# Kernel tuning notes

Hardware: AMD Instinct MI355X
Metric: run time of the kernel (lower is better)

## Reference

```python
import jax, jax.numpy as jnp
import numpy as np

GROUP = 128  # int4 quant group size and Hadamard block size

# Sylvester Hadamard matrix of size 128, orthonormal (H @ H.T = I)
_h = np.array([[1.0]], dtype=np.float32)
while _h.shape[0] < GROUP:
    _h = np.kron(_h, np.array([[1.0, 1.0], [1.0, -1.0]], dtype=np.float32))
H128 = jnp.asarray(_h / np.sqrt(GROUP))


def hadamard_rotate(x):
    # blockwise Hadamard rotation along the last dim (last dim % 128 == 0)
    *lead, n = x.shape
    xr = x.reshape(*lead, n // GROUP, GROUP) @ H128
    return xr.reshape(*lead, n)


def dequant_int4(wq, scales):
    # wq: [out, in] uint4 values in [0,16); scales: [out, in//GROUP]
    out_dim, in_dim = wq.shape
    w = (wq.astype(jnp.float32) - 8.0).reshape(out_dim, in_dim // GROUP, GROUP)
    w = w * scales[:, :, None]
    return w.reshape(out_dim, in_dim)


def rotate_linear_int4(x, wq, scales):
    # y = hadamard(x) @ dequant(W).T
    return hadamard_rotate(x) @ dequant_int4(wq, scales).T


def setup_inputs() -> dict:
    key = jax.random.key(0)
    ks = jax.random.split(key, 7)
    T, D, I = 4096, 4096, 12288  # tokens, hidden, intermediate
    x = jax.random.normal(ks[0], (T, D), dtype=jnp.float32)
    wq_gate = jax.random.randint(ks[1], (I, D), 0, 16, dtype=jnp.int32)
    s_gate = jax.random.uniform(ks[2], (I, D // GROUP), dtype=jnp.float32) * 0.01
    wq_up = jax.random.randint(ks[3], (I, D), 0, 16, dtype=jnp.int32)
    s_up = jax.random.uniform(ks[4], (I, D // GROUP), dtype=jnp.float32) * 0.01
    wq_down = jax.random.randint(ks[5], (D, I), 0, 16, dtype=jnp.int32)
    s_down = jax.random.uniform(ks[6], (D, I // GROUP), dtype=jnp.float32) * 0.01
    return {"x": x, "wq_gate": wq_gate, "s_gate": s_gate,
            "wq_up": wq_up, "s_up": s_up,
            "wq_down": wq_down, "s_down": s_down}


def reference(x, wq_gate, s_gate, wq_up, s_up, wq_down, s_down):
    gate = rotate_linear_int4(x, wq_gate, s_gate)   # [T, I]
    up = rotate_linear_int4(x, wq_up, s_up)         # [T, I]
    h = jax.nn.silu(gate) * up                       # SiluAndMul on cat([gate, up])
    return rotate_linear_int4(h, wq_down, s_down)    # [T, D]
```

## Files before the change

kernel.cpp:

```cpp
#include <hip/hip_runtime.h>
#include <hip/hip_bf16.h>
#include <cstdint>

#define T_DIM 4096
#define D_DIM 4096
#define I_DIM 12288
#define GRP   128

typedef __attribute__((ext_vector_type(8))) short bf16x8;
typedef __attribute__((ext_vector_type(4))) float f32x4;
typedef __attribute__((ext_vector_type(4))) int   int32x4;

typedef __attribute__((address_space(3))) void lds_void;
typedef const __attribute__((address_space(1))) void gmem_void;

static __device__ __forceinline__ unsigned short f2bf(float f) {
    unsigned int u = __float_as_uint(f);
    u += 0x7FFFu + ((u >> 16) & 1u);
    return (unsigned short)(u >> 16);
}
static __device__ __forceinline__ float bf2f(unsigned short b) {
    return __uint_as_float(((unsigned int)b) << 16);
}

__global__ void had_f32_to_bf16(const float* __restrict__ in, unsigned short* __restrict__ out,
                                int ngroups) {
    int gid = blockIdx.x * (blockDim.x >> 6) + (threadIdx.x >> 6);
    if (gid >= ngroups) return;
    int lane = threadIdx.x & 63;
    const float2 v2 = *reinterpret_cast<const float2*>(in + (size_t)gid * 128 + lane * 2);
    float v0 = v2.x, v1 = v2.y;
    { float t0 = v0 + v1, t1 = v0 - v1; v0 = t0; v1 = t1; }
#pragma unroll
    for (int m = 1; m <= 32; m <<= 1) {
        float b0 = __shfl_xor(v0, m);
        float b1 = __shfl_xor(v1, m);
        if (lane & m) { v0 = b0 - v0; v1 = b1 - v1; }
        else          { v0 = v0 + b0; v1 = v1 + b1; }
    }
    const float s = 0.08838834764831843f;
    unsigned int o = (unsigned int)f2bf(v0 * s) | ((unsigned int)f2bf(v1 * s) << 16);
    *reinterpret_cast<unsigned int*>(out + (size_t)gid * 128 + lane * 2) = o;
}

__global__ void had_bf16_inplace(unsigned short* __restrict__ buf, int ngroups) {
    int gid = blockIdx.x * (blockDim.x >> 6) + (threadIdx.x >> 6);
    if (gid >= ngroups) return;
    int lane = threadIdx.x & 63;
    unsigned int pv = *reinterpret_cast<const unsigned int*>(buf + (size_t)gid * 128 + lane * 2);
    float v0 = __uint_as_float((pv & 0xFFFFu) << 16);
    float v1 = __uint_as_float(pv & 0xFFFF0000u);
    { float t0 = v0 + v1, t1 = v0 - v1; v0 = t0; v1 = t1; }
#pragma unroll
    for (int m = 1; m <= 32; m <<= 1) {
        float b0 = __shfl_xor(v0, m);
        float b1 = __shfl_xor(v1, m);
        if (lane & m) { v0 = b0 - v0; v1 = b1 - v1; }
        else          { v0 = v0 + b0; v1 = v1 + b1; }
    }
    const float s = 0.08838834764831843f;
    unsigned int o = (unsigned int)f2bf(v0 * s) | ((unsigned int)f2bf(v1 * s) << 16);
    *reinterpret_cast<unsigned int*>(buf + (size_t)gid * 128 + lane * 2) = o;
}

__global__ void dequant_w(const int* __restrict__ Wq, const float* __restrict__ S,
                          unsigned short* __restrict__ Wbf, int In, int total8) {
    int t = blockIdx.x * blockDim.x + threadIdx.x;
    if (t >= total8) return;
    size_t base = (size_t)t * 8;
    size_t row = base / (size_t)In;
    int col = (int)(base - row * (size_t)In);
    float sc = S[row * (size_t)(In >> 7) + (col >> 7)];
    const int32x4* p = reinterpret_cast<const int32x4*>(Wq + base);
    int32x4 a = p[0], b = p[1];
    float nsc = -8.0f * sc;
    unsigned int o0 = (unsigned int)f2bf((float)a.x * sc + nsc) |
                      ((unsigned int)f2bf((float)a.y * sc + nsc) << 16);
    unsigned int o1 = (unsigned int)f2bf((float)a.z * sc + nsc) |
                      ((unsigned int)f2bf((float)a.w * sc + nsc) << 16);
    unsigned int o2 = (unsigned int)f2bf((float)b.x * sc + nsc) |
                      ((unsigned int)f2bf((float)b.y * sc + nsc) << 16);
    unsigned int o3 = (unsigned int)f2bf((float)b.z * sc + nsc) |
                      ((unsigned int)f2bf((float)b.w * sc + nsc) << 16);
    *reinterpret_cast<uint4*>(Wbf + base) = make_uint4(o0, o1, o2, o3);
}


#define GBAR()  __builtin_amdgcn_s_barrier()
#define FENCE() asm volatile("" ::: "memory")
#define VMW(n)  asm volatile("s_waitcnt vmcnt(" #n ")" ::: "memory")
#define P1()    __builtin_amdgcn_s_setprio(1)
#define P0()    __builtin_amdgcn_s_setprio(0)

#define STG(src, row0, base, h, kb)                                                    \
  { _Pragma("unroll")                                                                  \
    for (int i_ = 0; i_ < 2; ++i_) {                                                   \
      const int rl_ = (h) * 128 + i_ * 64 + (tid >> 3);                                \
      const int gs_ = (tid & 7) ^ ((tid >> 3) & 7);                                    \
      const unsigned short* gp_ = (src) + (size_t)((row0) + rl_) * K + (kb) + gs_ * 8; \
      unsigned short* lp_ = lds + (base) + ((h) * 128 + i_ * 64 + wid * 8) * 64;       \
      __builtin_amdgcn_global_load_lds((gmem_void*)gp_, (lds_void*)lp_, 16, 0, 0);     \
    } }

#define LDA(base, q)                                                                   \
  _Pragma("unroll")                                                                    \
  for (int mi_ = 0; mi_ < 2; ++mi_)                                                    \
  _Pragma("unroll")                                                                    \
  for (int ks_ = 0; ks_ < 2; ++ks_) {                                                  \
    int r_ = wr * 128 + (q) * 32 + mi_ * 16 + (lane & 15);                             \
    int c_ = ks_ * 4 + kc;                                                             \
    af[mi_][ks_] = *reinterpret_cast<const bf16x8*>(                                   \
        lds + (base) + r_ * 64 + ((c_ ^ (r_ & 7)) << 3));                              \
  }

#define LDB(base)                                                                      \
  _Pragma("unroll")                                                                    \
  for (int ni_ = 0; ni_ < 4; ++ni_)                                                    \
  _Pragma("unroll")                                                                    \
  for (int ks_ = 0; ks_ < 2; ++ks_) {                                                  \
    int r_ = wc * 64 + ni_ * 16 + (lane & 15);                                         \
    int c_ = ks_ * 4 + kc;                                                             \
    bk[ni_][ks_] = *reinterpret_cast<const bf16x8*>(                                   \
        lds + (base) + r_ * 64 + ((c_ ^ (r_ & 7)) << 3));                              \
  }

#define MF16(q)                                                                        \
  _Pragma("unroll")                                                                    \
  for (int ks_ = 0; ks_ < 2; ++ks_)                                                    \
  _Pragma("unroll")                                                                    \
  for (int mi_ = 0; mi_ < 2; ++mi_)                                                    \
  _Pragma("unroll")                                                                    \
  for (int ni_ = 0; ni_ < 4; ++ni_)                                                    \
    acc[(q) * 2 + mi_][ni_] = __builtin_amdgcn_mfma_f32_16x16x32_bf16(                 \
        af[mi_][ks_], bk[ni_][ks_], acc[(q) * 2 + mi_][ni_], 0, 0, 0);

#define B0_ 49152
#define B1_ 65536

template<int MODE>
__global__ __launch_bounds__(512, 2)
void gemm256(const unsigned short* __restrict__ A,
             const unsigned short* __restrict__ W,
             void* __restrict__ C, int M, int N, int K)
{
    __shared__ __align__(16) unsigned short lds[81920];

    const int MT = M >> 8;
    const int nwg = gridDim.x;
    const int bid = blockIdx.x;
    const int cpx = nwg >> 3;
    const int wg  = (bid & 7) * cpx + (bid >> 3);
    const int m0 = (wg % MT) << 8;
    const int n0 = (wg / MT) << 8;

    const int tid  = threadIdx.x;
    const int lane = tid & 63;
    const int wid  = tid >> 6;
    const int wr = wid >> 2;
    const int wc = wid & 3;
    const int kc = lane >> 4;

    f32x4 acc[8][4];
#pragma unroll
    for (int i = 0; i < 8; ++i)
#pragma unroll
        for (int j = 0; j < 4; ++j) acc[i][j] = (f32x4)0.0f;

    const int NT = K >> 6;
    const int J  = NT >> 1;

    STG(A, m0, 0,     0, 0);  STG(A, m0, 0,     1, 0);
    STG(W, n0, B0_,   0, 0);  STG(W, n0, B0_,   1, 0);
    STG(A, m0, 16384, 0, 64); STG(A, m0, 16384, 1, 64);
    STG(W, n0, B1_,   0, 64);
    VMW(6);
    GBAR(); FENCE();

    int ra = 0, rb = 1, rc = 2;

    for (int j = 0; j < J; ++j) {
        const bool st = (j < J - 1);
        const int a   = j << 1;
        const int kT1 = (a + 1) << 6;
        const int kT2 = (a + 2) << 6;
        const int kT3 = (a + 3) << 6;
        const int baA = ra << 14, bbA = rb << 14, bcA = rc << 14;
        bf16x8 af[2][2], bk[4][2];

        STG(W, n0, B1_, 1, kT1);
        LDB(B0_); LDA(baA, 0);
        P1(); MF16(0); P0(); GBAR(); FENCE();
        if (st) STG(A, m0, bcA, 0, kT2);
        LDA(baA, 1);
        P1(); MF16(1); P0(); GBAR(); FENCE();
        if (st) STG(W, n0, B0_, 0, kT2);
        LDA(baA, 2);
        P1(); MF16(2); P0(); GBAR(); FENCE();
        if (st) STG(W, n0, B0_, 1, kT2);
        LDA(baA, 3);
        P1(); MF16(3); P0();
        if (st) { VMW(6); } else { VMW(0); }
        GBAR(); FENCE();
        if (st) STG(A, m0, bcA, 1, kT2);
        LDB(B1_); LDA(bbA, 0);
        P1(); MF16(0); P0(); GBAR(); FENCE();
        if (st) STG(A, m0, baA, 0, kT3);
        LDA(bbA, 1);
        P1(); MF16(1); P0(); GBAR(); FENCE();
        if (st) STG(A, m0, baA, 1, kT3);
        LDA(bbA, 2);
        P1(); MF16(2); P0(); GBAR(); FENCE();
        if (st) STG(W, n0, B1_, 0, kT3);
        LDA(bbA, 3);
        P1(); MF16(3); P0();
        if (st) { VMW(6); }
        GBAR(); FENCE();
        int t_ = ra; ra = rc; rc = rb; rb = t_;
    }

#pragma unroll
    for (int mi = 0; mi < 8; ++mi)
#pragma unroll
        for (int ni = 0; ni < 4; ++ni) {
            const int col = n0 + (wc << 6) + ni * 16 + (lane & 15);
#pragma unroll
            for (int r = 0; r < 4; ++r) {
                const int row = m0 + (wr << 7) + mi * 16 + ((lane >> 4) << 2) + r;
                const size_t idx = (size_t)row * N + col;
                if (MODE == 2) {
                    ((float*)C)[idx] = acc[mi][ni][r];
                } else if (MODE == 0) {
                    ((unsigned short*)C)[idx] = f2bf(acc[mi][ni][r]);
                } else {
                    float g = bf2f(((unsigned short*)C)[idx]);
                    float u = acc[mi][ni][r];
                    float h = (g / (1.0f + __expf(-g))) * u;
                    ((unsigned short*)C)[idx] = f2bf(h);
                }
            }
        }
}

__global__ __launch_bounds__(256, 2)
void gemm_gateup_fb(const unsigned short* __restrict__ Xr,
                    const int* __restrict__ Wg, const float* __restrict__ Sg,
                    const int* __restrict__ Wu, const float* __restrict__ Su,
                    unsigned short* __restrict__ H)
{
    __shared__ __align__(16) unsigned short lA [128 * 64];
    __shared__ __align__(16) unsigned short lBg[128 * 64];
    __shared__ __align__(16) unsigned short lBu[128 * 64];
    const int MT = T_DIM / 128;
    const int bid = blockIdx.x;
    const int m0 = (bid % MT) * 128;
    const int n0 = (bid / MT) * 128;
    const int tid  = threadIdx.x;
    const int lane = tid & 63;
    const int wid  = tid >> 6;
    const int wr = wid >> 1, wc = wid & 1;
    f32x4 accG[4][4], accU[4][4];
#pragma unroll
    for (int i = 0; i < 4; ++i)
#pragma unroll
        for (int j = 0; j < 4; ++j) { accG[i][j] = (f32x4)0.0f; accU[i][j] = (f32x4)0.0f; }
    const int arow = lane >> 3;
    const int acol = (lane & 7) * 8;
    const int SStride = D_DIM / GRP;
    for (int k0 = 0; k0 < D_DIM; k0 += 64) {
        __syncthreads();
#pragma unroll
        for (int it = 0; it < 4; ++it) {
            int chunk = wid * 4 + it;
            const unsigned short* gp = Xr + (size_t)(m0 + chunk * 8 + arow) * D_DIM + k0 + acol;
            __builtin_amdgcn_global_load_lds((gmem_void*)gp, (lds_void*)(lA + chunk * 512), 16, 0, 0);
        }
        const int g = k0 >> 7;
#pragma unroll
        for (int i = 0; i < 8; ++i) {
            int linear = i * 1024 + tid * 4;
            int r = linear >> 6;
            int c = linear & 63;
            const int32x4 wg = *reinterpret_cast<const int32x4*>(Wg + (size_t)(n0 + r) * D_DIM + k0 + c);
            const int32x4 wu = *reinterpret_cast<const int32x4*>(Wu + (size_t)(n0 + r) * D_DIM + k0 + c);
            float scg = Sg[(size_t)(n0 + r) * SStride + g];
            float scu = Su[(size_t)(n0 + r) * SStride + g];
            unsigned int g01 = (unsigned int)f2bf((float)(wg.x - 8) * scg) | ((unsigned int)f2bf((float)(wg.y - 8) * scg) << 16);
            unsigned int g23 = (unsigned int)f2bf((float)(wg.z - 8) * scg) | ((unsigned int)f2bf((float)(wg.w - 8) * scg) << 16);
            unsigned int u01 = (unsigned int)f2bf((float)(wu.x - 8) * scu) | ((unsigned int)f2bf((float)(wu.y - 8) * scu) << 16);
            unsigned int u23 = (unsigned int)f2bf((float)(wu.z - 8) * scu) | ((unsigned int)f2bf((float)(wu.w - 8) * scu) << 16);
            *reinterpret_cast<uint2*>(lBg + r * 64 + c) = make_uint2(g01, g23);
            *reinterpret_cast<uint2*>(lBu + r * 64 + c) = make_uint2(u01, u23);
        }
        __syncthreads();
#pragma unroll
        for (int ks = 0; ks < 2; ++ks) {
            const int koff = ks * 32 + (lane >> 4) * 8;
            bf16x8 af[4], bg[4], bu[4];
#pragma unroll
            for (int mi = 0; mi < 4; ++mi)
                af[mi] = *reinterpret_cast<const bf16x8*>(lA + (wr * 64 + mi * 16 + (lane & 15)) * 64 + koff);
#pragma unroll
            for (int ni = 0; ni < 4; ++ni) {
                bg[ni] = *reinterpret_cast<const bf16x8*>(lBg + (wc * 64 + ni * 16 + (lane & 15)) * 64 + koff);
                bu[ni] = *reinterpret_cast<const bf16x8*>(lBu + (wc * 64 + ni * 16 + (lane & 15)) * 64 + koff);
            }
#pragma unroll
            for (int mi = 0; mi < 4; ++mi)
#pragma unroll
                for (int ni = 0; ni < 4; ++ni) {
                    accG[mi][ni] = __builtin_amdgcn_mfma_f32_16x16x32_bf16(af[mi], bg[ni], accG[mi][ni], 0, 0, 0);
                    accU[mi][ni] = __builtin_amdgcn_mfma_f32_16x16x32_bf16(af[mi], bu[ni], accU[mi][ni], 0, 0, 0);
                }
        }
    }
#pragma unroll
    for (int mi = 0; mi < 4; ++mi)
#pragma unroll
        for (int ni = 0; ni < 4; ++ni) {
            const int col = n0 + wc * 64 + ni * 16 + (lane & 15);
#pragma unroll
            for (int r = 0; r < 4; ++r) {
                const int row = m0 + wr * 64 + mi * 16 + (lane >> 4) * 4 + r;
                float gv = accG[mi][ni][r];
                float uv = accU[mi][ni][r];
                float hv = (gv / (1.0f + __expf(-gv))) * uv;
                H[(size_t)row * I_DIM + col] = f2bf(hv);
            }
        }
}

__global__ __launch_bounds__(256, 2)
void gemm_down_fb(const unsigned short* __restrict__ Hr,
                  const int* __restrict__ Wd, const float* __restrict__ Sd,
                  float* __restrict__ Out)
{
    __shared__ __align__(16) unsigned short lA[128 * 64];
    __shared__ __align__(16) unsigned short lB[128 * 64];
    const int MT = T_DIM / 128;
    const int bid = blockIdx.x;
    const int m0 = (bid % MT) * 128;
    const int n0 = (bid / MT) * 128;
    const int tid  = threadIdx.x;
    const int lane = tid & 63;
    const int wid  = tid >> 6;
    const int wr = wid >> 1, wc = wid & 1;
    f32x4 acc[4][4];
#pragma unroll
    for (int i = 0; i < 4; ++i)
#pragma unroll
        for (int j = 0; j < 4; ++j) acc[i][j] = (f32x4)0.0f;
    const int arow = lane >> 3;
    const int acol = (lane & 7) * 8;
    const int SStride = I_DIM / GRP;
    for (int k0 = 0; k0 < I_DIM; k0 += 64) {
        __syncthreads();
#pragma unroll
        for (int it = 0; it < 4; ++it) {
            int chunk = wid * 4 + it;
            const unsigned short* gp = Hr + (size_t)(m0 + chunk * 8 + arow) * I_DIM + k0 + acol;
            __builtin_amdgcn_global_load_lds((gmem_void*)gp, (lds_void*)(lA + chunk * 512), 16, 0, 0);
        }
        const int g = k0 >> 7;
#pragma unroll
        for (int i = 0; i < 8; ++i) {
            int linear = i * 1024 + tid * 4;
            int r = linear >> 6;
            int c = linear & 63;
            const int32x4 wd = *reinterpret_cast<const int32x4*>(Wd + (size_t)(n0 + r) * I_DIM + k0 + c);
            float sc = Sd[(size_t)(n0 + r) * SStride + g];
            unsigned int d01 = (unsigned int)f2bf((float)(wd.x - 8) * sc) | ((unsigned int)f2bf((float)(wd.y - 8) * sc) << 16);
            unsigned int d23 = (unsigned int)f2bf((float)(wd.z - 8) * sc) | ((unsigned int)f2bf((float)(wd.w - 8) * sc) << 16);
            *reinterpret_cast<uint2*>(lB + r * 64 + c) = make_uint2(d01, d23);
        }
        __syncthreads();
#pragma unroll
        for (int ks = 0; ks < 2; ++ks) {
            const int koff = ks * 32 + (lane >> 4) * 8;
            bf16x8 af[4], bfr[4];
#pragma unroll
            for (int mi = 0; mi < 4; ++mi)
                af[mi] = *reinterpret_cast<const bf16x8*>(lA + (wr * 64 + mi * 16 + (lane & 15)) * 64 + koff);
#pragma unroll
            for (int ni = 0; ni < 4; ++ni)
                bfr[ni] = *reinterpret_cast<const bf16x8*>(lB + (wc * 64 + ni * 16 + (lane & 15)) * 64 + koff);
#pragma unroll
            for (int mi = 0; mi < 4; ++mi)
#pragma unroll
                for (int ni = 0; ni < 4; ++ni)
                    acc[mi][ni] = __builtin_amdgcn_mfma_f32_16x16x32_bf16(af[mi], bfr[ni], acc[mi][ni], 0, 0, 0);
        }
    }
#pragma unroll
    for (int mi = 0; mi < 4; ++mi)
#pragma unroll
        for (int ni = 0; ni < 4; ++ni) {
            const int col = n0 + wc * 64 + ni * 16 + (lane & 15);
#pragma unroll
            for (int r = 0; r < 4; ++r) {
                const int row = m0 + wr * 64 + mi * 16 + (lane >> 4) * 4 + r;
                Out[(size_t)row * D_DIM + col] = acc[mi][ni][r];
            }
        }
}

extern "C" void kernel_launch(void* const* d_in, const int* in_sizes, int n_in,
                              void* d_out, int out_size, void* d_ws, size_t ws_size,
                              hipStream_t stream) {
    const float* x       = (const float*)d_in[0];
    const int*   wq_gate = (const int*)d_in[1];
    const float* s_gate  = (const float*)d_in[2];
    const int*   wq_up   = (const int*)d_in[3];
    const float* s_up    = (const float*)d_in[4];
    const int*   wq_down = (const int*)d_in[5];
    const float* s_down  = (const float*)d_in[6];
    float* out = (float*)d_out;

    const size_t XR_E = (size_t)T_DIM * D_DIM;
    const size_t H_E  = (size_t)T_DIM * I_DIM;
    const size_t W_E  = (size_t)I_DIM * D_DIM;
    const size_t need = (XR_E + H_E + 2 * W_E) * sizeof(unsigned short);

    unsigned short* xr = (unsigned short*)d_ws;
    unsigned short* h  = xr + XR_E;

    {
        int ngroups = (int)(XR_E / 128);
        had_f32_to_bf16<<<dim3(ngroups / 4), dim3(256), 0, stream>>>(x, xr, ngroups);
    }

    if (ws_size >= need) {
        unsigned short* wgbf = h + H_E;
        unsigned short* wubf = wgbf + W_E;
        int total8 = (int)(W_E / 8);
        dequant_w<<<dim3((total8 + 255) / 256), dim3(256), 0, stream>>>(wq_gate, s_gate, wgbf, D_DIM, total8);
        dequant_w<<<dim3((total8 + 255) / 256), dim3(256), 0, stream>>>(wq_up,   s_up,   wubf, D_DIM, total8);
        gemm256<0><<<dim3((T_DIM / 256) * (I_DIM / 256)), dim3(512), 0, stream>>>(
            xr, wgbf, (void*)h, T_DIM, I_DIM, D_DIM);
        gemm256<1><<<dim3((T_DIM / 256) * (I_DIM / 256)), dim3(512), 0, stream>>>(
            xr, wubf, (void*)h, T_DIM, I_DIM, D_DIM);
        {
            int ngroups = (int)(H_E / 128);
            had_bf16_inplace<<<dim3(ngroups / 4), dim3(256), 0, stream>>>(h, ngroups);
        }
        dequant_w<<<dim3((total8 + 255) / 256), dim3(256), 0, stream>>>(wq_down, s_down, wgbf, I_DIM, total8);
        gemm256<2><<<dim3((T_DIM / 256) * (D_DIM / 256)), dim3(512), 0, stream>>>(
            h, wgbf, (void*)out, T_DIM, D_DIM, I_DIM);
    } else {
        gemm_gateup_fb<<<dim3((T_DIM / 128) * (I_DIM / 128)), dim3(256), 0, stream>>>(
            xr, wq_gate, s_gate, wq_up, s_up, h);
        {
            int ngroups = (int)(H_E / 128);
            had_bf16_inplace<<<dim3(ngroups / 4), dim3(256), 0, stream>>>(h, ngroups);
        }
        gemm_down_fb<<<dim3((T_DIM / 128) * (D_DIM / 128)), dim3(256), 0, stream>>>(
            h, wq_down, s_down, out);
    }
}
```

Measured before the change: 1.302 ms.

## Double-buffer LDS-to-register fragments to overlap ds_reads with MFMA in GEMM

Restructures the GEMM main loop so A and B register fragments are double-buffered (afA/afB, bkA/bkB). The next sub-tile's LDS reads are issued before the current MFMA block, with explicit lgkmcnt waits and sched_barriers. The global-to-LDS staging schedule is re-timed: prologue loads one more stage, and the final iteration is peeled into an epilogue to drop per-iteration conditionals. The aim is to hide LDS read latency behind matrix math, at the cost of more VGPRs, which may strain the 2-waves-per-SIMD launch bound, and of subtle correctness risk in the reworked buffer rotation.

After: 2.571 ms. 1.97x slower.

```diff
diff --git a/kernel.cpp b/kernel.cpp
--- a/kernel.cpp
+++ b/kernel.cpp
@@ -86,11 +86,12 @@
 }
 
 
-#define GBAR()  __builtin_amdgcn_s_barrier()
-#define FENCE() asm volatile("" ::: "memory")
-#define VMW(n)  asm volatile("s_waitcnt vmcnt(" #n ")" ::: "memory")
-#define P1()    __builtin_amdgcn_s_setprio(1)
-#define P0()    __builtin_amdgcn_s_setprio(0)
+#define GBAR()   __builtin_amdgcn_s_barrier()
+#define LGKM(n)  asm volatile("s_waitcnt lgkmcnt(" #n ")" ::: "memory")
+#define VMW(n)   asm volatile("s_waitcnt vmcnt(" #n ")" ::: "memory")
+#define SB0()    __builtin_amdgcn_sched_barrier(0)
+#define P1()     __builtin_amdgcn_s_setprio(1)
+#define P0()     __builtin_amdgcn_s_setprio(0)
 
 #define STG(src, row0, base, h, kb)                                                    \
   { _Pragma("unroll")                                                                  \
@@ -102,29 +103,29 @@
       __builtin_amdgcn_global_load_lds((gmem_void*)gp_, (lds_void*)lp_, 16, 0, 0);     \
     } }
 
-#define LDA(base, q)                                                                   \
+#define LDA(dst, base, q)                                                              \
   _Pragma("unroll")                                                                    \
   for (int mi_ = 0; mi_ < 2; ++mi_)                                                    \
   _Pragma("unroll")                                                                    \
   for (int ks_ = 0; ks_ < 2; ++ks_) {                                                  \
     int r_ = wr * 128 + (q) * 32 + mi_ * 16 + (lane & 15);                             \
     int c_ = ks_ * 4 + kc;                                                             \
-    af[mi_][ks_] = *reinterpret_cast<const bf16x8*>(                                   \
+    dst[mi_][ks_] = *reinterpret_cast<const bf16x8*>(                                  \
         lds + (base) + r_ * 64 + ((c_ ^ (r_ & 7)) << 3));                              \
   }
 
-#define LDB(base)                                                                      \
+#define LDB(dst, base)                                                                 \
   _Pragma("unroll")                                                                    \
   for (int ni_ = 0; ni_ < 4; ++ni_)                                                    \
   _Pragma("unroll")                                                                    \
   for (int ks_ = 0; ks_ < 2; ++ks_) {                                                  \
     int r_ = wc * 64 + ni_ * 16 + (lane & 15);                                         \
     int c_ = ks_ * 4 + kc;                                                             \
-    bk[ni_][ks_] = *reinterpret_cast<const bf16x8*>(                                   \
+    dst[ni_][ks_] = *reinterpret_cast<const bf16x8*>(                                  \
         lds + (base) + r_ * 64 + ((c_ ^ (r_ & 7)) << 3));                              \
   }
 
-#define MF16(q)                                                                        \
+#define MF16(q, afb, bkb)                                                              \
   _Pragma("unroll")                                                                    \
   for (int ks_ = 0; ks_ < 2; ++ks_)                                                    \
   _Pragma("unroll")                                                                    \
@@ -132,7 +133,7 @@
   _Pragma("unroll")                                                                    \
   for (int ni_ = 0; ni_ < 4; ++ni_)                                                    \
     acc[(q) * 2 + mi_][ni_] = __builtin_amdgcn_mfma_f32_16x16x32_bf16(                 \
-        af[mi_][ks_], bk[ni_][ks_], acc[(q) * 2 + mi_][ni_], 0, 0, 0);
+        afb[mi_][ks_], bkb[ni_][ks_], acc[(q) * 2 + mi_][ni_], 0, 0, 0);
 
 #define B0_ 49152
 #define B1_ 65536
@@ -169,53 +170,103 @@
     const int NT = K >> 6;
     const int J  = NT >> 1;
 
-    STG(A, m0, 0,     0, 0);  STG(A, m0, 0,     1, 0);
-    STG(W, n0, B0_,   0, 0);  STG(W, n0, B0_,   1, 0);
+    bf16x8 afA[2][2], afB[2][2], bkA[4][2], bkB[4][2];
+
+    STG(A, m0, 0, 0, 0);     STG(A, m0, 0, 1, 0);
+    STG(W, n0, B0_, 0, 0);   STG(W, n0, B0_, 1, 0);
+    VMW(0);
+    GBAR();
+    LDB(bkA, B0_);
+    LDA(afA, 0, 0);
     STG(A, m0, 16384, 0, 64); STG(A, m0, 16384, 1, 64);
-    STG(W, n0, B1_,   0, 64);
-    VMW(6);
-    GBAR(); FENCE();
+    STG(W, n0, B1_, 0, 64);   STG(W, n0, B1_, 1, 64);
+    STG(A, m0, 32768, 0, 128);
+    GBAR();
 
     int ra = 0, rb = 1, rc = 2;
 
-    for (int j = 0; j < J; ++j) {
-        const bool st = (j < J - 1);
+    for (int j = 0; j < J - 1; ++j) {
         const int a   = j << 1;
-        const int kT1 = (a + 1) << 6;
         const int kT2 = (a + 2) << 6;
         const int kT3 = (a + 3) << 6;
+        const int kT4 = (a + 4) << 6;
         const int baA = ra << 14, bbA = rb << 14, bcA = rc << 14;
-        bf16x8 af[2][2], bk[4][2];
-
-        STG(W, n0, B1_, 1, kT1);
-        LDB(B0_); LDA(baA, 0);
-        P1(); MF16(0); P0(); GBAR(); FENCE();
-        if (st) STG(A, m0, bcA, 0, kT2);
-        LDA(baA, 1);
-        P1(); MF16(1); P0(); GBAR(); FENCE();
-        if (st) STG(W, n0, B0_, 0, kT2);
-        LDA(baA, 2);
-        P1(); MF16(2); P0(); GBAR(); FENCE();
-        if (st) STG(W, n0, B0_, 1, kT2);
-        LDA(baA, 3);
-        P1(); MF16(3); P0();
-        if (st) { VMW(6); } else { VMW(0); }
-        GBAR(); FENCE();
-        if (st) STG(A, m0, bcA, 1, kT2);
-        LDB(B1_); LDA(bbA, 0);
-        P1(); MF16(0); P0(); GBAR(); FENCE();
-        if (st) STG(A, m0, baA, 0, kT3);
-        LDA(bbA, 1);
-        P1(); MF16(1); P0(); GBAR(); FENCE();
-        if (st) STG(A, m0, baA, 1, kT3);
-        LDA(bbA, 2);
-        P1(); MF16(2); P0(); GBAR(); FENCE();
-        if (st) STG(W, n0, B1_, 0, kT3);
-        LDA(bbA, 3);
-        P1(); MF16(3); P0();
-        if (st) { VMW(6); }
-        GBAR(); FENCE();
+
+        LDA(afB, baA, 1);
+        LGKM(4); SB0();
+        P1(); MF16(0, afA, bkA); P0();
+        STG(W, n0, B0_, 0, kT2);
+        GBAR();
+        LDA(afA, baA, 2);
+        LGKM(4); SB0();
+        P1(); MF16(1, afB, bkA); P0();
+        STG(W, n0, B0_, 1, kT2);
+        GBAR();
+        LDA(afB, baA, 3);
+        LGKM(4); SB0();
+        P1(); MF16(2, afA, bkA); P0();
+        STG(A, m0, bcA, 1, kT2);
+        VMW(6);
+        GBAR();
+        LDB(bkB, B1_);
+        LDA(afA, bbA, 0);
+        LGKM(12); SB0();
+        P1(); MF16(3, afB, bkA); P0();
+        STG(A, m0, baA, 0, kT3);
+        GBAR();
+        LDA(afB, bbA, 1);
+        LGKM(4); SB0();
+        P1(); MF16(0, afA, bkB); P0();
+        STG(A, m0, baA, 1, kT3);
+        GBAR();
+        LDA(afA, bbA, 2);
+        LGKM(4); SB0();
+        P1(); MF16(1, afB, bkB); P0();
+        STG(W, n0, B1_, 0, kT3);
+        GBAR();
+        LDA(afB, bbA, 3);
+        LGKM(4); SB0();
+        P1(); MF16(2, afA, bkB); P0();
+        STG(W, n0, B1_, 1, kT3);
+        VMW(6);
+        GBAR();
+        LDB(bkA, B0_);
+        LDA(afA, bcA, 0);
+        LGKM(12); SB0();
+        P1(); MF16(3, afB, bkB); P0();
+        if (j < J - 2) { STG(A, m0, bbA, 0, kT4); }
+        GBAR();
         int t_ = ra; ra = rc; rc = rb; rb = t_;
+    }
+
+    {
+        const int baA = ra << 14, bbA = rb << 14;
+        LDA(afB, baA, 1);
+        LGKM(4); SB0();
+        P1(); MF16(0, afA, bkA); P0(); GBAR();
+        LDA(afA, baA, 2);
+        LGKM(4); SB0();
+        P1(); MF16(1, afB, bkA); P0(); GBAR();
+        LDA(afB, baA, 3);
+        LGKM(4); SB0();
+        P1(); MF16(2, afA, bkA); P0();
+        VMW(0);
+        GBAR();
+        LDB(bkB, B1_);
+        LDA(afA, bbA, 0);
+        LGKM(12); SB0();
+        P1(); MF16(3, afB, bkA); P0(); GBAR();
+        LDA(afB, bbA, 1);
+        LGKM(4); SB0();
+        P1(); MF16(0, afA, bkB); P0(); GBAR();
+        LDA(afA, bbA, 2);
+        LGKM(4); SB0();
+        P1(); MF16(1, afB, bkB); P0(); GBAR();
+        LDA(afB, bbA, 3);
+        LGKM(4); SB0();
+        P1(); MF16(2, afA, bkB); P0(); GBAR();
+        LGKM(0); SB0();
+        P1(); MF16(3, afB, bkB); P0();
     }
 
 #pragma unroll
```
